# Kernel optimization log

Hardware: AMD Instinct MI355X
Metric: run time of the kernel (lower is better)

## Reference

```python
import jax, jax.numpy as jnp
import numpy as np

D_MODEL = 1024
N_HEADS = 16
D_HEAD = D_MODEL // N_HEADS
B, T = 2, 2048
EPS = 1e-5


def setup_inputs() -> dict:
    key = jax.random.key(0)
    ks = jax.random.split(key, 5)
    s = 1.0 / np.sqrt(D_MODEL)
    return {
        "x": jax.random.normal(ks[0], (B, T, D_MODEL), dtype=jnp.float32),
        "W_q": jax.random.normal(ks[1], (D_MODEL, D_MODEL), dtype=jnp.float32) * s,
        "W_k": jax.random.normal(ks[2], (D_MODEL, D_MODEL), dtype=jnp.float32) * s,
        "W_v": jax.random.normal(ks[3], (D_MODEL, D_MODEL), dtype=jnp.float32) * s,
        "W_o": jax.random.normal(ks[4], (D_MODEL, D_MODEL), dtype=jnp.float32) * s,
        "gn_weight": jnp.ones((D_MODEL,), dtype=jnp.float32),
        "gn_bias": jnp.zeros((D_MODEL,), dtype=jnp.float32),
    }


def reference(x, W_q, W_k, W_v, W_o, gn_weight, gn_bias):
    b, t, dm = x.shape
    h, dh = N_HEADS, D_HEAD
    # per-head decay factors gamma_i = 1 - 2^(-5-i)
    gammas = 1.0 - 2.0 ** (-5.0 - jnp.arange(h, dtype=jnp.float32))  # [H]

    # projections (torch Linear: y = x @ W.T), split heads -> [B,T,H,Dh]
    q = (x @ W_q.T).reshape(b, t, h, dh)
    k = (x @ W_k.T).reshape(b, t, h, dh)
    v = (x @ W_v.T).reshape(b, t, h, dh)

    # causal decay mask D[h,i,j] = gamma_h^(i-j) for i>=j else 0
    idx = jnp.arange(t)
    diff = idx[:, None] - idx[None, :]                      # [T,T]
    pow_ = jnp.maximum(diff, 0).astype(jnp.float32)
    decay = jnp.where(diff >= 0, gammas[:, None, None] ** pow_, 0.0)  # [H,T,T]

    scale = jnp.sqrt(jnp.float32(dh))
    attn = jnp.einsum('bihd,bjhd->bhij', q, k) * decay[None] / scale  # [B,H,T,T]
    y = jnp.einsum('bhij,bjhd->bihd', attn, v)               # [B,T,H,Dh]

    # GroupNorm(n_heads, d_model) over channels-first layout: per (b, head)
    # normalize over (T, d_head)
    mean = y.mean(axis=(1, 3), keepdims=True)
    var = y.var(axis=(1, 3), keepdims=True)
    yn = (y - mean) / jnp.sqrt(var + EPS)
    yn = yn.reshape(b, t, dm) * gn_weight + gn_bias

    return yn @ W_o.T
```

## Files before the change

### kernel.cpp

```cpp
#include <hip/hip_runtime.h>
#include <stdint.h>


#define SEQ 2048

typedef __bf16 bf16x8 __attribute__((ext_vector_type(8)));
typedef float  floatx4 __attribute__((ext_vector_type(4)));
typedef unsigned short ushort4v __attribute__((ext_vector_type(4)));

__device__ __forceinline__ unsigned short f2bf(float f){
    __bf16 h = (__bf16)f;
    return __builtin_bit_cast(unsigned short, h);
}

__device__ __forceinline__ void gload_lds16(const void* g, void* l){
    __builtin_amdgcn_global_load_lds(
        (const __attribute__((address_space(1))) unsigned int*)g,
        (__attribute__((address_space(3))) unsigned int*)l, 16, 0, 0);
}

__global__ __launch_bounds__(256)
void cvt_all(const float* __restrict__ x,
             const float* __restrict__ w0, const float* __restrict__ w1,
             const float* __restrict__ w2, const float* __restrict__ w3,
             unsigned short* __restrict__ xb,
             unsigned short* __restrict__ o0, unsigned short* __restrict__ o1,
             unsigned short* __restrict__ o2, unsigned short* __restrict__ o3,
             float* __restrict__ st){
    const int blk = blockIdx.x;
    if(blk == 0 && threadIdx.x < 128) st[threadIdx.x] = 0.0f;
    const float* src; unsigned short* dst; size_t i;
    if(blk < 4096){ src = x; dst = xb; i = (size_t)blk*256 + threadIdx.x; }
    else {
        const int seg = (blk - 4096) >> 10;
        src = seg==0?w0:seg==1?w1:seg==2?w2:w3;
        dst = seg==0?o0:seg==1?o1:seg==2?o2:o3;
        i = (size_t)((blk - 4096) & 1023)*256 + threadIdx.x;
    }
    float4 v = ((const float4*)src)[i];
    ushort4v o;
    o[0]=f2bf(v.x); o[1]=f2bf(v.y); o[2]=f2bf(v.z); o[3]=f2bf(v.w);
    *(ushort4v*)&dst[i*4] = o;
}

__global__ __launch_bounds__(256, 3)
void gemm_qkv(const unsigned short* __restrict__ A,
              const unsigned short* __restrict__ Wq,
              const unsigned short* __restrict__ Wk,
              const unsigned short* __restrict__ Wv,
              unsigned short* __restrict__ Qo,
              unsigned short* __restrict__ Ko,
              unsigned short* __restrict__ Vo)
{
    __shared__ unsigned short smem[16384];
    unsigned short* As = smem;
    unsigned short* Bs = smem + 4096;
    const int tid  = threadIdx.x;
    const int w    = tid >> 6, lane = tid & 63, q = lane >> 4, cl = lane & 15;
    const int i0   = blockIdx.x * 128;
    const int ysel = blockIdx.y;
    int mode, n0;
    const unsigned short* Bw;
    unsigned short* O;
    if(ysel < 8)      { mode = 0; Bw = Wq; O = Qo; n0 = ysel*128; }
    else if(ysel < 16){ mode = 1; Bw = Wk; O = Ko; n0 = (ysel-8)*128; }
    else              { mode = 2; Bw = Wv; O = Vo; n0 = (ysel-16)*128; }
    const int wm = (w & 1) * 64, wn = (w >> 1) * 64;

    floatx4 acc[4][4];
    #pragma unroll
    for(int a=0;a<4;a++)
        #pragma unroll
        for(int b=0;b<4;b++) acc[a][b] = (floatx4)(0.0f);

    const int srow = lane >> 2;
    const int soff = (lane & 3) * 16;

    for(int k0 = 0; k0 < 1024; k0 += 32){
        __syncthreads();
        #pragma unroll
        for(int t=0;t<2;t++){
            const int ra = (w*2 + t) * 16;
            gload_lds16((const char*)A  + ((size_t)(i0 + ra + srow)*1024 + k0)*2 + soff,
                        (char*)&As[ra*32]);
            gload_lds16((const char*)Bw + ((size_t)(n0 + ra + srow)*1024 + k0)*2 + soff,
                        (char*)&Bs[ra*32]);
        }
        __syncthreads();

        bf16x8 af[4], bfr[4];
        #pragma unroll
        for(int mi=0;mi<4;mi++) af[mi]  = *(const bf16x8*)&As[(wm + mi*16 + cl)*32 + q*8];
        #pragma unroll
        for(int ni=0;ni<4;ni++) bfr[ni] = *(const bf16x8*)&Bs[(wn + ni*16 + cl)*32 + q*8];
        #pragma unroll
        for(int mi=0;mi<4;mi++)
            #pragma unroll
            for(int ni=0;ni<4;ni++)
                acc[mi][ni] = __builtin_amdgcn_mfma_f32_16x16x32_bf16(af[mi], bfr[ni], acc[mi][ni], 0, 0, 0);
    }

    const int b = i0 >> 11;
    const int tb = i0 & 2047;
    __syncthreads();

    if(mode < 2){
        const int h = (n0 + wn) >> 6;
        const float gamma = 1.0f - __builtin_ldexpf(1.0f, -5 - h);
        const float lgh = log2f(gamma);
        float g1p, base;
        if(mode == 0){ g1p = gamma;        base = exp2f((float)tb * lgh) * 0.125f; }
        else         { g1p = 1.0f / gamma; base = exp2f(-(float)tb * lgh); }
        const float g2 = g1p*g1p, g4 = g2*g2, g8 = g4*g4, g16 = g8*g8;
        const float g32 = g16*g16, g64 = g32*g32;
        float sq = base;
        if(q & 1) sq *= g4;
        if(q & 2) sq *= g8;
        if(wm)    sq *= g64;

        #pragma unroll
        for(int ni=0;ni<4;ni++){
            const int d = wn + ni*16 + cl, d8 = d >> 3, d7 = d & 7;
            float cur = sq;
            #pragma unroll
            for(int mi=0;mi<4;mi++){
                const int tr0 = wm + mi*16 + q*4;
                float v0 = cur, v1 = v0*g1p, v2 = v1*g1p, v3 = v2*g1p;
                smem[(tr0+0)*128 + ((d8 ^ ((tr0+0)&7))*8) + d7] = f2bf(acc[mi][ni][0]*v0);
                smem[(tr0+1)*128 + ((d8 ^ ((tr0+1)&7))*8) + d7] = f2bf(acc[mi][ni][1]*v1);
                smem[(tr0+2)*128 + ((d8 ^ ((tr0+2)&7))*8) + d7] = f2bf(acc[mi][ni][2]*v2);
                smem[(tr0+3)*128 + ((d8 ^ ((tr0+3)&7))*8) + d7] = f2bf(acc[mi][ni][3]*v3);
                cur *= g16;
            }
        }
        __syncthreads();
        const int part = tid & 3;
        #pragma unroll
        for(int rr=0;rr<2;rr++){
            const int row = (tid>>2)*2 + rr;
            const int tt = tb + row;
            #pragma unroll
            for(int k=0;k<4;k++){
                const int c = k*4 + part;
                bf16x8 vrow = *(const bf16x8*)&smem[row*128 + ((c ^ (row&7))*8)];
                const int h2 = (n0 + c*8) >> 6, dd = (c*8) & 63;
                *(bf16x8*)&O[(((size_t)(b*16 + h2))*2048 + tt)*64 + dd] = vrow;
            }
        }
    } else {
        #pragma unroll
        for(int ni=0;ni<4;ni++){
            const int drow = wn + ni*16 + cl, dr7 = drow & 7;
            #pragma unroll
            for(int mi=0;mi<4;mi++){
                const int ch = (wm>>3) + mi*2 + (q>>1);
                const int phys = (ch & 8) | ((ch & 7) ^ dr7);
                ushort4v pk;
                #pragma unroll
                for(int r=0;r<4;r++) pk[r] = f2bf(acc[mi][ni][r]);
                *(ushort4v*)&smem[drow*128 + phys*8 + (q&1)*4] = pk;
            }
        }
        __syncthreads();
        const int part = tid & 3;
        #pragma unroll
        for(int rr=0;rr<2;rr++){
            const int row = (tid>>2)*2 + rr;
            const int dg = n0 + row;
            const int h2 = dg >> 6, dd = dg & 63;
            #pragma unroll
            for(int k=0;k<4;k++){
                const int c = k*4 + part;
                const int phys = (c & 8) | ((c & 7) ^ (row & 7));
                bf16x8 vrow = *(const bf16x8*)&smem[row*128 + phys*8];
                *(bf16x8*)&O[(((size_t)(b*16 + h2))*64 + dd)*2048 + tb + c*8] = vrow;
            }
        }
    }
}

__global__ __launch_bounds__(256, 2)
void retention(const unsigned short* __restrict__ Q,
               const unsigned short* __restrict__ K,
               const unsigned short* __restrict__ VT,
               float* __restrict__ Y0, float* __restrict__ Y1)
{
    __shared__ unsigned short Ks[2][64*64];
    __shared__ unsigned short Vs[2][64*64];
    __shared__ unsigned short Ss[4][32*64];

    const int tid = threadIdx.x;
    const int w = tid >> 6, lane = tid & 63, q = lane >> 4, cl = lane & 15;
    const int s = blockIdx.x >> 3, x = blockIdx.x & 7;
    const int bh = blockIdx.y;
    const int wm = w * 32;
    const int l3 = lane >> 3, l7 = lane & 7;
    const int c8 = l7 ^ l3;
    const int cl7 = cl & 7;

    bf16x8 qf[2][2];
    floatx4 Yacc[2][4];

    auto entry = [&](int e, int& bt, int& jloc){
        if(s == 0){
            if(e <= 2*x+1){ bt = x;    jloc = e; }
            else          { bt = 15-x; jloc = e - (2*x+2); }
        } else            { bt = 15-x; jloc = e + 15 - 2*x; }
    };

    auto stage = [&](int p, int j0){
        #pragma unroll
        for(int t=0;t<2;t++){
            const int r = w*16 + t*8 + l3;
            gload_lds16((const char*)K  + (((size_t)bh*SEQ + j0 + r)*64 + c8*8)*2,
                        (char*)&Ks[p][(w*16 + t*8)*64]);
            gload_lds16((const char*)VT + (((size_t)bh*64 + r)*SEQ + j0 + c8*8)*2,
                        (char*)&Vs[p][(w*16 + t*8)*64]);
        }
    };

    auto flushf = [&](int bt_f){
        const int i0f = bt_f*128;
        #pragma unroll
        for(int mi=0;mi<2;mi++)
            #pragma unroll
            for(int nt=0;nt<4;nt++){
                const int ig = i0f + wm + mi*16 + cl;
                #pragma unroll
                for(int r=0;r<4;r++){
                    const int d = nt*16 + q*4 + r;
                    if(s == 0)
                        Y0[((size_t)bh*64 + d)*2048 + ig] = Yacc[mi][nt][r];
                    else
                        Y1[((size_t)bh*64 + d)*1024 + ig - 1024] = Yacc[mi][nt][r];
                }
            }
    };

    {
        int bt0, jl0; entry(0, bt0, jl0);
        stage(0, jl0*64);
    }

    int cur_bt = -1;
    int p = 0;
    for(int e = 0; e < 17; e++){
        int bt, jloc; entry(e, bt, jloc);
        const int i0 = bt*128, j0 = jloc*64;

        if(bt != cur_bt){
            if(cur_bt >= 0) flushf(cur_bt);
            #pragma unroll
            for(int mi=0;mi<2;mi++)
                #pragma unroll
                for(int kk=0;kk<2;kk++)
                    qf[mi][kk] = *(const bf16x8*)(Q + ((size_t)bh*SEQ + i0 + wm + mi*16 + cl)*64 + kk*32 + q*8);
            #pragma unroll
            for(int a=0;a<2;a++)
                #pragma unroll
                for(int b=0;b<4;b++) Yacc[a][b] = (floatx4)(0.0f);
            cur_bt = bt;
        }

        __syncthreads();
        if(e < 16){ int btn, jln; entry(e+1, btn, jln); stage(p^1, jln*64); }

        const unsigned short* KsP = Ks[p];
        const unsigned short* VsP = Vs[p];

        floatx4 St[2][4];
        #pragma unroll
        for(int a=0;a<2;a++)
            #pragma unroll
            for(int b=0;b<4;b++) St[a][b] = (floatx4)(0.0f);
        #pragma unroll
        for(int kk=0;kk<2;kk++){
            #pragma unroll
            for(int ni=0;ni<4;ni++){
                bf16x8 ak = *(const bf16x8*)&KsP[(ni*16 + cl)*64 + ((kk*4+q) ^ cl7)*8];
                St[0][ni] = __builtin_amdgcn_mfma_f32_16x16x32_bf16(ak, qf[0][kk], St[0][ni], 0,0,0);
                St[1][ni] = __builtin_amdgcn_mfma_f32_16x16x32_bf16(ak, qf[1][kk], St[1][ni], 0,0,0);
            }
        }

        const bool need_mask = (jloc >= 2*bt);
        unsigned short* SsW = Ss[w];
        #pragma unroll
        for(int mi=0;mi<2;mi++){
            const int row = mi*16 + cl;
            const int sw = row & 7;
            const int ig = i0 + wm + row;
            #pragma unroll
            for(int ni=0;ni<4;ni++){
                ushort4v pk;
                #pragma unroll
                for(int r=0;r<4;r++){
                    float v = St[mi][ni][r];
                    if(need_mask){
                        const int jg = j0 + ni*16 + q*4 + r;
                        if(ig < jg) v = 0.0f;
                    }
                    pk[r] = f2bf(v);
                }
                *(ushort4v*)&SsW[row*64 + (((ni*2 + (q>>1)) ^ sw)*8) + (q&1)*4] = pk;
            }
        }
        asm volatile("s_waitcnt lgkmcnt(0)" ::: "memory");

        #pragma unroll
        for(int kk=0;kk<2;kk++){
            const int ch = ((kk*4+q) ^ cl7)*8;
            bf16x8 bs0 = *(const bf16x8*)&SsW[( 0 + cl)*64 + ch];
            bf16x8 bs1 = *(const bf16x8*)&SsW[(16 + cl)*64 + ch];
            #pragma unroll
            for(int nt=0;nt<4;nt++){
                bf16x8 av = *(const bf16x8*)&VsP[(nt*16 + cl)*64 + ch];
                Yacc[0][nt] = __builtin_amdgcn_mfma_f32_16x16x32_bf16(av, bs0, Yacc[0][nt], 0,0,0);
                Yacc[1][nt] = __builtin_amdgcn_mfma_f32_16x16x32_bf16(av, bs1, Yacc[1][nt], 0,0,0);
            }
        }
        p ^= 1;
    }
    flushf(cur_bt);
}

__global__ __launch_bounds__(256)
void gn_stats(const float* __restrict__ Y0, const float* __restrict__ Y1,
              float* __restrict__ st){
    const int g = blockIdx.x >> 3, s8 = blockIdx.x & 7;
    if(g >= 32) return;
    float s1 = 0.f, s2 = 0.f;
    #pragma unroll
    for(int it=0; it<16; it++){
        const int idx = it*256 + threadIdx.x;
        const int dl = idx >> 9;
        const int t4 = idx & 511;
        const int drow = g*64 + s8*8 + dl;
        float4 v = ((const float4*)Y0)[(size_t)drow*512 + t4];
        if(t4 >= 256){
            float4 u = ((const float4*)Y1)[(size_t)drow*256 + t4 - 256];
            v.x += u.x; v.y += u.y; v.z += u.z; v.w += u.w;
        }
        s1 += v.x + v.y + v.z + v.w;
        s2 += v.x*v.x + v.y*v.y + v.z*v.z + v.w*v.w;
    }
    #pragma unroll
    for(int o=32;o>0;o>>=1){ s1 += __shfl_down(s1,o); s2 += __shfl_down(s2,o); }
    __shared__ float r1[4], r2[4];
    const int w = threadIdx.x >> 6, lane = threadIdx.x & 63;
    if(lane == 0){ r1[w] = s1; r2[w] = s2; }
    __syncthreads();
    if(threadIdx.x == 0){
        atomicAdd(&st[g*2+0], r1[0]+r1[1]+r1[2]+r1[3]);
        atomicAdd(&st[g*2+1], r2[0]+r2[1]+r2[2]+r2[3]);
    }
}

__global__ __launch_bounds__(256)
void gn_norm(const float* __restrict__ Y0, const float* __restrict__ Y1,
             const float* __restrict__ st,
             const float* __restrict__ gw, const float* __restrict__ gb,
             unsigned short* __restrict__ Out){
    __shared__ unsigned short T[64*72];
    const int g = blockIdx.x >> 5;
    if(g >= 32) return;
    const int t0 = (blockIdx.x & 31) * 64;
    const int h = g & 15, b = g >> 4;
    const float mean = st[g*2+0] * (1.0f/131072.0f);
    const float var  = st[g*2+1] * (1.0f/131072.0f) - mean*mean;
    const float inv  = rsqrtf(var + 1e-5f);
    const int tid = threadIdx.x;
    const bool hi = (t0 >= 1024);
    #pragma unroll
    for(int kk=0;kk<4;kk++){
        const int f4 = kk*256 + tid;
        const int d = f4 >> 4;
        const int t4l = f4 & 15;
        float4 v = ((const float4*)Y0)[(size_t)(g*64 + d)*512 + (t0>>2) + t4l];
        if(hi){
            float4 u = ((const float4*)Y1)[(size_t)(g*64 + d)*256 + ((t0-1024)>>2) + t4l];
            v.x += u.x; v.y += u.y; v.z += u.z; v.w += u.w;
        }
        const int c = h*64 + d;
        const float sc = inv * gw[c];
        const float bs = gb[c] - mean*sc;
        const int tl = t4l*4;
        T[(tl+0)*72 + d] = f2bf(v.x*sc + bs);
        T[(tl+1)*72 + d] = f2bf(v.y*sc + bs);
        T[(tl+2)*72 + d] = f2bf(v.z*sc + bs);
        T[(tl+3)*72 + d] = f2bf(v.w*sc + bs);
    }
    __syncthreads();
    #pragma unroll
    for(int it=0; it<2; it++){
        const int idx = it*256 + tid;
        const int tl = idx >> 3, segp = idx & 7;
        bf16x8 vrow = *(const bf16x8*)&T[tl*72 + segp*8];
        *(bf16x8*)&Out[((size_t)(b*2048 + t0 + tl))*1024 + h*64 + segp*8] = vrow;
    }
}

__global__ __launch_bounds__(256, 3)
void gemm_out(const unsigned short* __restrict__ A,
              const unsigned short* __restrict__ Bw,
              float* __restrict__ O)
{
    __shared__ unsigned short As[128*32];
    __shared__ unsigned short Bs[64*32];
    const int tid = threadIdx.x;
    const int w = tid >> 6, lane = tid & 63, q = lane >> 4, cl = lane & 15;
    const int i0 = blockIdx.x * 128, n0 = blockIdx.y * 64;
    const int wm = (w & 1) * 64, wn = (w >> 1) * 32;

    floatx4 acc[4][2];
    #pragma unroll
    for(int a=0;a<4;a++)
        #pragma unroll
        for(int b=0;b<2;b++) acc[a][b] = (floatx4)(0.0f);

    const int srow = lane >> 2;
    const int soff = (lane & 3) * 16;

    for(int k0 = 0; k0 < 1024; k0 += 32){
        __syncthreads();
        #pragma unroll
        for(int t=0;t<2;t++){
            const int ra = w*32 + t*16;
            gload_lds16((const char*)A + ((size_t)(i0 + ra + srow)*1024 + k0)*2 + soff,
                        (char*)&As[ra*32]);
        }
        gload_lds16((const char*)Bw + ((size_t)(n0 + w*16 + srow)*1024 + k0)*2 + soff,
                    (char*)&Bs[(w*16)*32]);
        __syncthreads();

        bf16x8 af[4], bfr[2];
        #pragma unroll
        for(int mi=0;mi<4;mi++) af[mi]  = *(const bf16x8*)&As[(wm + mi*16 + cl)*32 + q*8];
        #pragma unroll
        for(int ni=0;ni<2;ni++) bfr[ni] = *(const bf16x8*)&Bs[(wn + ni*16 + cl)*32 + q*8];
        #pragma unroll
        for(int mi=0;mi<4;mi++)
            #pragma unroll
            for(int ni=0;ni<2;ni++)
                acc[mi][ni] = __builtin_amdgcn_mfma_f32_16x16x32_bf16(af[mi], bfr[ni], acc[mi][ni], 0, 0, 0);
    }

    #pragma unroll
    for(int mi=0;mi<4;mi++)
        #pragma unroll
        for(int ni=0;ni<2;ni++){
            const int gi = i0 + wm + mi*16 + q*4;
            const int gn = n0 + wn + ni*16 + cl;
            #pragma unroll
            for(int r=0;r<4;r++) O[(size_t)(gi + r)*1024 + gn] = acc[mi][ni][r];
        }
}

extern "C" void kernel_launch(void* const* d_in, const int* in_sizes, int n_in,
                              void* d_out, int out_size, void* d_ws, size_t ws_size,
                              hipStream_t stream){
    const float* x  = (const float*)d_in[0];
    const float* Wq = (const float*)d_in[1];
    const float* Wk = (const float*)d_in[2];
    const float* Wv = (const float*)d_in[3];
    const float* Wo = (const float*)d_in[4];
    const float* gw = (const float*)d_in[5];
    const float* gb = (const float*)d_in[6];

    char* ws = (char*)d_ws;
    unsigned short* xb  = (unsigned short*)(ws + ((size_t) 0<<20));
    unsigned short* wqb = (unsigned short*)(ws + ((size_t) 8<<20));
    unsigned short* wkb = (unsigned short*)(ws + ((size_t)10<<20));
    unsigned short* wvb = (unsigned short*)(ws + ((size_t)12<<20));
    unsigned short* wob = (unsigned short*)(ws + ((size_t)14<<20));
    unsigned short* qb  = (unsigned short*)(ws + ((size_t)16<<20));
    unsigned short* kb  = (unsigned short*)(ws + ((size_t)24<<20));
    unsigned short* vtb = (unsigned short*)(ws + ((size_t)32<<20));
    float*          y0  = (float*)         (ws + ((size_t)40<<20));
    unsigned short* ynb = (unsigned short*)(ws + ((size_t)56<<20));
    float*          y1  = (float*)         (ws + ((size_t) 0<<20));
    float*          st  = (float*)         (ws + ((size_t)64<<20));

    cvt_all<<<8192, 256, 0, stream>>>(x, Wq, Wk, Wv, Wo, xb, wqb, wkb, wvb, wob, st);

    gemm_qkv<<<dim3(32,24,1), 256, 0, stream>>>(xb, wqb, wkb, wvb, qb, kb, vtb);

    retention<<<dim3(16,32,1), 256, 0, stream>>>(qb, kb, vtb, y0, y1);

    gn_stats<<<256, 256, 0, stream>>>(y0, y1, st);
    gn_norm<<<1024, 256, 0, stream>>>(y0, y1, st, gw, gb, ynb);

    gemm_out<<<dim3(32,16,1), 256, 0, stream>>>(ynb, wob, (float*)d_out);
}
```

Measured before the change: 186.5 us.

## Split causal retention work evenly into 24 runs per head with atomic accumulation

```diff
diff --git a/kernel.cpp b/kernel.cpp
--- a/kernel.cpp
+++ b/kernel.cpp
@@ -26,9 +26,14 @@
              unsigned short* __restrict__ xb,
              unsigned short* __restrict__ o0, unsigned short* __restrict__ o1,
              unsigned short* __restrict__ o2, unsigned short* __restrict__ o3,
-             float* __restrict__ st){
+             float* __restrict__ y0, float* __restrict__ st){
     const int blk = blockIdx.x;
     if(blk == 0 && threadIdx.x < 128) st[threadIdx.x] = 0.0f;
+    if(blk >= 8192){
+        float4 z = {0.f,0.f,0.f,0.f};
+        ((float4*)y0)[(size_t)(blk - 8192)*256 + threadIdx.x] = z;
+        return;
+    }
     const float* src; unsigned short* dst; size_t i;
     if(blk < 4096){ src = x; dst = xb; i = (size_t)blk*256 + threadIdx.x; }
     else {
@@ -179,11 +184,11 @@
     }
 }
 
-__global__ __launch_bounds__(256, 2)
+__global__ __launch_bounds__(256, 3)
 void retention(const unsigned short* __restrict__ Q,
                const unsigned short* __restrict__ K,
                const unsigned short* __restrict__ VT,
-               float* __restrict__ Y0, float* __restrict__ Y1)
+               float* __restrict__ Y0)
 {
     __shared__ unsigned short Ks[2][64*64];
     __shared__ unsigned short Vs[2][64*64];
@@ -191,22 +196,22 @@
 
     const int tid = threadIdx.x;
     const int w = tid >> 6, lane = tid & 63, q = lane >> 4, cl = lane & 15;
-    const int s = blockIdx.x >> 3, x = blockIdx.x & 7;
+    const int run = blockIdx.x;
     const int bh = blockIdx.y;
     const int wm = w * 32;
     const int l3 = lane >> 3, l7 = lane & 7;
     const int c8 = l7 ^ l3;
     const int cl7 = cl & 7;
 
+    const int e0 = (run < 8) ? run*12 : 96 + (run-8)*11;
+    const int e1 = (run < 8) ? e0+12  : e0+11;
+
+    int bt = 0;
+    while((bt+1)*(bt+2) <= e0) bt++;
+    int jloc = e0 - (bt*bt + bt);
+
     bf16x8 qf[2][2];
     floatx4 Yacc[2][4];
-
-    auto entry = [&](int e, int& bt, int& jloc){
-        if(s == 0){
-            if(e <= 2*x+1){ bt = x;    jloc = e; }
-            else          { bt = 15-x; jloc = e - (2*x+2); }
-        } else            { bt = 15-x; jloc = e + 15 - 2*x; }
-    };
 
     auto stage = [&](int p, int j0){
         #pragma unroll
@@ -229,23 +234,16 @@
                 #pragma unroll
                 for(int r=0;r<4;r++){
                     const int d = nt*16 + q*4 + r;
-                    if(s == 0)
-                        Y0[((size_t)bh*64 + d)*2048 + ig] = Yacc[mi][nt][r];
-                    else
-                        Y1[((size_t)bh*64 + d)*1024 + ig - 1024] = Yacc[mi][nt][r];
+                    atomicAdd(&Y0[((size_t)bh*64 + d)*2048 + ig], Yacc[mi][nt][r]);
                 }
             }
     };
 
-    {
-        int bt0, jl0; entry(0, bt0, jl0);
-        stage(0, jl0*64);
-    }
+    stage(0, jloc*64);
 
     int cur_bt = -1;
     int p = 0;
-    for(int e = 0; e < 17; e++){
-        int bt, jloc; entry(e, bt, jloc);
+    for(int e = e0; e < e1; e++){
         const int i0 = bt*128, j0 = jloc*64;
 
         if(bt != cur_bt){
@@ -263,7 +261,9 @@
         }
 
         __syncthreads();
-        if(e < 16){ int btn, jln; entry(e+1, btn, jln); stage(p^1, jln*64); }
+        int btn = bt, jln = jloc + 1;
+        if(jln == 2*btn + 2){ btn++; jln = 0; }
+        if(e + 1 < e1) stage(p^1, jln*64);
 
         const unsigned short* KsP = Ks[p];
         const unsigned short* VsP = Vs[p];
@@ -320,13 +320,13 @@
             }
         }
         p ^= 1;
+        bt = btn; jloc = jln;
     }
     flushf(cur_bt);
 }
 
 __global__ __launch_bounds__(256)
-void gn_stats(const float* __restrict__ Y0, const float* __restrict__ Y1,
-              float* __restrict__ st){
+void gn_stats(const float* __restrict__ Y0, float* __restrict__ st){
     const int g = blockIdx.x >> 3, s8 = blockIdx.x & 7;
     if(g >= 32) return;
     float s1 = 0.f, s2 = 0.f;
@@ -337,10 +337,6 @@
         const int t4 = idx & 511;
         const int drow = g*64 + s8*8 + dl;
         float4 v = ((const float4*)Y0)[(size_t)drow*512 + t4];
-        if(t4 >= 256){
-            float4 u = ((const float4*)Y1)[(size_t)drow*256 + t4 - 256];
-            v.x += u.x; v.y += u.y; v.z += u.z; v.w += u.w;
-        }
         s1 += v.x + v.y + v.z + v.w;
         s2 += v.x*v.x + v.y*v.y + v.z*v.z + v.w*v.w;
     }
@@ -357,8 +353,7 @@
 }
 
 __global__ __launch_bounds__(256)
-void gn_norm(const float* __restrict__ Y0, const float* __restrict__ Y1,
-             const float* __restrict__ st,
+void gn_norm(const float* __restrict__ Y0, const float* __restrict__ st,
              const float* __restrict__ gw, const float* __restrict__ gb,
              unsigned short* __restrict__ Out){
     __shared__ unsigned short T[64*72];
@@ -370,17 +365,12 @@
     const float var  = st[g*2+1] * (1.0f/131072.0f) - mean*mean;
     const float inv  = rsqrtf(var + 1e-5f);
     const int tid = threadIdx.x;
-    const bool hi = (t0 >= 1024);
     #pragma unroll
     for(int kk=0;kk<4;kk++){
         const int f4 = kk*256 + tid;
         const int d = f4 >> 4;
         const int t4l = f4 & 15;
         float4 v = ((const float4*)Y0)[(size_t)(g*64 + d)*512 + (t0>>2) + t4l];
-        if(hi){
-            float4 u = ((const float4*)Y1)[(size_t)(g*64 + d)*256 + ((t0-1024)>>2) + t4l];
-            v.x += u.x; v.y += u.y; v.z += u.z; v.w += u.w;
-        }
         const int c = h*64 + d;
         const float sc = inv * gw[c];
         const float bs = gb[c] - mean*sc;
@@ -478,17 +468,16 @@
     unsigned short* vtb = (unsigned short*)(ws + ((size_t)32<<20));
     float*          y0  = (float*)         (ws + ((size_t)40<<20));
     unsigned short* ynb = (unsigned short*)(ws + ((size_t)56<<20));
-    float*          y1  = (float*)         (ws + ((size_t) 0<<20));
     float*          st  = (float*)         (ws + ((size_t)64<<20));
 
-    cvt_all<<<8192, 256, 0, stream>>>(x, Wq, Wk, Wv, Wo, xb, wqb, wkb, wvb, wob, st);
+    cvt_all<<<12288, 256, 0, stream>>>(x, Wq, Wk, Wv, Wo, xb, wqb, wkb, wvb, wob, y0, st);
 
     gemm_qkv<<<dim3(32,24,1), 256, 0, stream>>>(xb, wqb, wkb, wvb, qb, kb, vtb);
 
-    retention<<<dim3(16,32,1), 256, 0, stream>>>(qb, kb, vtb, y0, y1);
-
-    gn_stats<<<256, 256, 0, stream>>>(y0, y1, st);
-    gn_norm<<<1024, 256, 0, stream>>>(y0, y1, st, gw, gb, ynb);
+    retention<<<dim3(24,32,1), 256, 0, stream>>>(qb, kb, vtb, y0);
+
+    gn_stats<<<256, 256, 0, stream>>>(y0, st);
+    gn_norm<<<1024, 256, 0, stream>>>(y0, st, gw, gb, ynb);
 
     gemm_out<<<dim3(32,16,1), 256, 0, stream>>>(ynb, wob, (float*)d_out);
 }
```

After: 197.4 us. 1.06x slower.
